# Kernel tuning notes

Measured on AMD Instinct MI355X. Metric: run time of the kernel, lower is better.

The kernel has to match this reference:

```python
import jax, jax.numpy as jnp
import numpy as np

B, N, D_IN, D_OUT = 8, 2048, 256, 256
BN_EPS = 1e-5
SELU_ALPHA = 1.6732632423543772
SELU_SCALE = 1.0507009873554805


def setup_inputs() -> dict:
    key = jax.random.key(0)
    k1, k2, k3, k4 = jax.random.split(key, 4)
    lim_lin = 1.0 / np.sqrt(D_IN)
    return {
        "x": jax.random.normal(k1, (B, N, D_IN), dtype=jnp.float32),
        "w_map": jax.random.uniform(k2, (D_IN,), jnp.float32, -lim_lin, lim_lin),
        "w_att": jax.random.uniform(k3, (D_OUT, D_IN), jnp.float32, -lim_lin, lim_lin),
        "w_res": jax.random.uniform(k4, (D_OUT, D_IN), jnp.float32, -lim_lin, lim_lin),
        "gamma": jnp.ones((D_OUT,), jnp.float32),
        "beta": jnp.zeros((D_OUT,), jnp.float32),
    }


def _selu(x):
    x_clamped = jnp.clip(x, -10.0, 10.0)
    return SELU_SCALE * jnp.where(x > 0, x, SELU_ALPHA * (jnp.exp(x_clamped) - 1.0))


def reference(x, w_map, w_att, w_res, gamma, beta):
    # scores[b,i,j] = sum_d w_map[d] * x[b,i,d] * x[b,j,d]  (== W_map(x_i*x_j))
    scores = jnp.einsum("bid,bjd->bij", x * w_map, x)  # [B,N,N]
    attn = jax.nn.softmax(scores, axis=-1)
    aggregated = jnp.einsum("bij,bjd->bid", attn, x)  # [B,N,D]
    out = aggregated @ w_att.T + x @ w_res.T  # [B,N,D_OUT]
    # BatchNorm1d in training mode: stats over (batch, nodes) per channel, biased var
    mean = jnp.mean(out, axis=(0, 1))
    var = jnp.mean(jnp.square(out - mean), axis=(0, 1))
    out = (out - mean) * jax.lax.rsqrt(var + BN_EPS) * gamma + beta
    return _selu(out)
```

## Files before the change

kernel.cpp:

```cpp
#include <hip/hip_runtime.h>
#include <hip/hip_bf16.h>


typedef __attribute__((ext_vector_type(8))) short  bf16x8;
typedef __attribute__((ext_vector_type(4))) float  f32x4;

#define MFMA16(a, b, c) __builtin_amdgcn_mfma_f32_16x16x32_bf16((a), (b), (c), 0, 0, 0)

constexpr int   NB = 8, NN = 2048, ND = 256;
constexpr int   ROWS = NB * NN;
constexpr float BN_EPS = 1e-5f;
constexpr float SELU_ALPHA = 1.6732632423543772f;
constexpr float SELU_SCALE = 1.0507009873554805f;

__device__ __forceinline__ unsigned short f2bf(float f) {
  union { float f; unsigned int u; } v; v.f = f;
  unsigned int u = v.u;
  u += 0x7FFFu + ((u >> 16) & 1u);
  return (unsigned short)(u >> 16);
}
__device__ __forceinline__ float bf2f(unsigned short h) {
  union { float f; unsigned int u; } v; v.u = ((unsigned int)h) << 16;
  return v.f;
}

__device__ __forceinline__ void async_copy16(const unsigned short* g, unsigned short* l) {
  __builtin_amdgcn_global_load_lds(
      (const __attribute__((address_space(1))) void*)g,
      (__attribute__((address_space(3))) void*)l, 16, 0, 0);
}

__global__ __launch_bounds__(256) void k0_prep(const float* __restrict__ x,
                                               const float* __restrict__ w_att,
                                               const float* __restrict__ w_res,
                                               unsigned short* __restrict__ Xr,
                                               unsigned short* __restrict__ Xt,
                                               unsigned short* __restrict__ WC,
                                               float* __restrict__ sums) {
  __shared__ unsigned short Ls[32 * 264];
  const int t = threadIdx.x;
  if (blockIdx.x >= 512) {
    const int bid = blockIdx.x - 512;
    if (bid == 0 && t < 128)
      ((float4*)sums)[t] = make_float4(0.f, 0.f, 0.f, 0.f);
    int f = (bid * 256 + t) * 8;
    int c = f >> 9, k = f & 511;
    const float* src = (k < 256) ? (w_att + c * 256 + k) : (w_res + c * 256 + (k - 256));
    float4 a = *(const float4*)src;
    float4 b = *(const float4*)(src + 4);
    union { unsigned short s[8]; uint4 v; } o;
    o.s[0] = f2bf(a.x); o.s[1] = f2bf(a.y); o.s[2] = f2bf(a.z); o.s[3] = f2bf(a.w);
    o.s[4] = f2bf(b.x); o.s[5] = f2bf(b.y); o.s[6] = f2bf(b.z); o.s[7] = f2bf(b.w);
    *(uint4*)(WC + f) = o.v;
    return;
  }
  const int b = blockIdx.x & 7, rt = blockIdx.x >> 3;
  const int grb = b * NN + rt * 32;
  const int c = (t & 31) * 8, r0 = t >> 5;
#pragma unroll
  for (int q = 0; q < 4; ++q) {
    int r = r0 + q * 8;
    const float* xp = x + (size_t)(grb + r) * 256 + c;
    float4 a = *(const float4*)xp;
    float4 d = *(const float4*)(xp + 4);
    union { unsigned short s[8]; uint4 v; } xb;
    xb.s[0] = f2bf(a.x); xb.s[1] = f2bf(a.y); xb.s[2] = f2bf(a.z); xb.s[3] = f2bf(a.w);
    xb.s[4] = f2bf(d.x); xb.s[5] = f2bf(d.y); xb.s[6] = f2bf(d.z); xb.s[7] = f2bf(d.w);
    *(uint4*)(Xr + (size_t)(grb + r) * 256 + c) = xb.v;
    *(uint4*)&Ls[r * 264 + c] = xb.v;
  }
  __syncthreads();
  unsigned short* dst = Xt + ((size_t)b * 256 + t) * 2048 + rt * 32;
#pragma unroll
  for (int k = 0; k < 4; ++k) {
    union { unsigned short s[8]; uint4 v; } o;
#pragma unroll
    for (int j = 0; j < 8; ++j) o.s[j] = Ls[(k * 8 + j) * 264 + t];
    *(uint4*)(dst + k * 8) = o.v;
  }
}

__global__ __launch_bounds__(512, 2) void k1_attn(const float* __restrict__ w_map,
                                                  const unsigned short* __restrict__ Xr,
                                                  const unsigned short* __restrict__ Xt,
                                                  const unsigned short* __restrict__ WC,
                                                  float* __restrict__ out,
                                                  float* __restrict__ sums) {
  __shared__ unsigned short Ks[2][2][32 * 256];
  __shared__ unsigned short Vt[2][2][256 * 32];
  __shared__ unsigned short Psw[8][16 * 40];
  __shared__ float Lb[64];

  const int t = threadIdx.x;
  const int w = t >> 6, lane = t & 63, l15 = lane & 15, quad = lane >> 4;
  const int g = w >> 2, wg = w & 3;
  const int b = blockIdx.x & 7, it = blockIdx.x >> 3;
  const int gib = b * NN + it * 64;
  const unsigned short* Xtb = Xt + (size_t)b * 256 * 2048;
  const unsigned short* Xrb = Xr + (size_t)b * NN * 256;
  const int jgbase = g * 1024;

  int ksOff[4], vtOff[4];
#pragma unroll
  for (int q = 0; q < 4; ++q) {
    int j = wg * 8 + q * 2 + (lane >> 5);
    int ck = (lane & 31) ^ (j & 7);
    ksOff[q] = j * 256 + ck * 8;
    int d = wg * 64 + q * 16 + (lane >> 2);
    int cv = (lane & 3) ^ ((d >> 1) & 3);
    vtOff[q] = d * 2048 + cv * 8;
  }
  const int ldsOff = wg * 2048 + lane * 8;

  bf16x8 qf[8];
  {
    const unsigned short* xrow = Xrb + (size_t)(it * 64 + wg * 16 + l15) * 256;
#pragma unroll
    for (int kc = 0; kc < 8; ++kc) {
      bf16x8 xb = *(const bf16x8*)(xrow + kc * 32 + quad * 8);
      const float* wp = w_map + kc * 32 + quad * 8;
      float4 w0 = *(const float4*)wp, w1 = *(const float4*)(wp + 4);
      float wv[8] = {w0.x, w0.y, w0.z, w0.w, w1.x, w1.y, w1.z, w1.w};
      bf16x8 q;
#pragma unroll
      for (int i = 0; i < 8; ++i)
        q[i] = (short)f2bf(bf2f((unsigned short)xb[i]) * wv[i]);
      qf[kc] = q;
    }
  }

  const f32x4 fz = {0.f, 0.f, 0.f, 0.f};
  f32x4 oacc[16];
#pragma unroll
  for (int i = 0; i < 16; ++i) oacc[i] = fz;
  f32x4 oL = fz;

  bf16x8 onesFrag;
  {
    short o1 = (l15 == 0) ? (short)0x3F80 : (short)0;
#pragma unroll
    for (int i = 0; i < 8; ++i) onesFrag[i] = o1;
  }

#pragma unroll
  for (int q = 0; q < 4; ++q)
    async_copy16(Xrb + (size_t)jgbase * 256 + ksOff[q], &Ks[g][0][ldsOff + q * 512]);
#pragma unroll
  for (int q = 0; q < 4; ++q)
    async_copy16(Xtb + jgbase + vtOff[q], &Vt[g][0][ldsOff + q * 512]);

  for (int jt = 0; jt < 32; ++jt) {
    const int cur = jt & 1;
    __syncthreads();
    if (jt < 31) {
      const int jb1 = jgbase + (jt + 1) * 32;
#pragma unroll
      for (int q = 0; q < 4; ++q)
        async_copy16(Xrb + (size_t)jb1 * 256 + ksOff[q], &Ks[g][cur ^ 1][ldsOff + q * 512]);
#pragma unroll
      for (int q = 0; q < 4; ++q)
        async_copy16(Xtb + jb1 + vtOff[q], &Vt[g][cur ^ 1][ldsOff + q * 512]);
    }
#pragma unroll
    for (int jm = 0; jm < 2; ++jm) {
      const int j = jm * 16 + l15;
      f32x4 s = fz;
#pragma unroll
      for (int kc = 0; kc < 8; ++kc) {
        int ckk = kc * 4 + quad;
        bf16x8 kf = *(const bf16x8*)&Ks[g][cur][j * 256 + ((ckk ^ (j & 7)) * 8)];
        s = MFMA16(kf, qf[kc], s);
      }
      ushort4 pk;
      pk.x = f2bf(__expf(s[0])); pk.y = f2bf(__expf(s[1]));
      pk.z = f2bf(__expf(s[2])); pk.w = f2bf(__expf(s[3]));
      *(ushort4*)&Psw[w][l15 * 40 + jm * 16 + quad * 4] = pk;
    }
    bf16x8 af = *(const bf16x8*)&Psw[w][l15 * 40 + quad * 8];
#pragma unroll
    for (int nti = 0; nti < 16; ++nti) {
      const int d = nti * 16 + l15;
      bf16x8 vf = *(const bf16x8*)&Vt[g][cur][d * 32 + ((quad ^ ((d >> 1) & 3)) * 8)];
      oacc[nti] = MFMA16(af, vf, oacc[nti]);
    }
    oL = MFMA16(af, onesFrag, oL);
  }

  __syncthreads();
  float* Obuf = (float*)&Ks[0][0][0];
  unsigned short* Agg = &Vt[0][0][0];
  if (g == 1) {
#pragma unroll
    for (int nti = 0; nti < 16; ++nti)
#pragma unroll
      for (int r = 0; r < 4; ++r) {
        int row = quad * 4 + r;
        Obuf[wg * 4096 + row * 256 + (((nti + quad) & 15) << 4) + l15] = oacc[nti][r];
      }
    if (l15 == 0) {
#pragma unroll
      for (int r = 0; r < 4; ++r) Lb[wg * 16 + quad * 4 + r] = oL[r];
    }
  }
  __syncthreads();
  if (g == 0) {
    float ls[4];
#pragma unroll
    for (int r = 0; r < 4; ++r) ls[r] = Lb[wg * 16 + quad * 4 + r];
#pragma unroll
    for (int nti = 0; nti < 16; ++nti)
#pragma unroll
      for (int r = 0; r < 4; ++r) {
        int row = quad * 4 + r;
        oacc[nti][r] += Obuf[wg * 4096 + row * 256 + (((nti + quad) & 15) << 4) + l15];
      }
    float li[4];
#pragma unroll
    for (int r = 0; r < 4; ++r)
      li[r] = 1.0f / (__shfl(oL[r], lane & 48) + ls[r]);
#pragma unroll
    for (int nti = 0; nti < 16; ++nti)
#pragma unroll
      for (int r = 0; r < 4; ++r)
        Agg[(wg * 16 + quad * 4 + r) * 264 + nti * 16 + l15] =
            f2bf(oacc[nti][r] * li[r]);
  }
  __syncthreads();

  f32x4 eacc[2][4];
#pragma unroll
  for (int i = 0; i < 2; ++i)
#pragma unroll
    for (int j = 0; j < 4; ++j) eacc[i][j] = fz;

#pragma unroll
  for (int kc = 0; kc < 16; ++kc) {
    bf16x8 bf0 = *(const bf16x8*)(WC + (size_t)(w * 32 + l15) * 512 + kc * 32 + quad * 8);
    bf16x8 bf1 = *(const bf16x8*)(WC + (size_t)(w * 32 + 16 + l15) * 512 + kc * 32 + quad * 8);
#pragma unroll
    for (int rt = 0; rt < 4; ++rt) {
      bf16x8 af;
      if (kc < 8)
        af = *(const bf16x8*)&Agg[(rt * 16 + l15) * 264 + kc * 32 + quad * 8];
      else
        af = *(const bf16x8*)(Xrb + (size_t)(it * 64 + rt * 16 + l15) * 256 +
                              (kc - 8) * 32 + quad * 8);
      eacc[0][rt] = MFMA16(af, bf0, eacc[0][rt]);
      eacc[1][rt] = MFMA16(af, bf1, eacc[1][rt]);
    }
  }
#pragma unroll
  for (int nt = 0; nt < 2; ++nt) {
    float a = 0.f, b2 = 0.f;
#pragma unroll
    for (int rt = 0; rt < 4; ++rt)
#pragma unroll
      for (int r = 0; r < 4; ++r) {
        float v = eacc[nt][rt][r];
        a += v; b2 += v * v;
      }
    a += __shfl_xor(a, 16);  a += __shfl_xor(a, 32);
    b2 += __shfl_xor(b2, 16); b2 += __shfl_xor(b2, 32);
    if (quad == 0) {
      int ci = w * 32 + nt * 16 + l15;
      atomicAdd(&sums[ci], a);
      atomicAdd(&sums[256 + ci], b2);
    }
  }
#pragma unroll
  for (int nt = 0; nt < 2; ++nt) {
    const int gcol = w * 32 + nt * 16 + l15;
#pragma unroll
    for (int rt = 0; rt < 4; ++rt)
#pragma unroll
      for (int r = 0; r < 4; ++r) {
        const int grow = gib + rt * 16 + quad * 4 + r;
        out[(size_t)grow * 256 + gcol] = eacc[nt][rt][r];
      }
  }
}

__global__ __launch_bounds__(256) void k4_bn_selu(float* __restrict__ out,
                                                  const float* __restrict__ sums,
                                                  const float* __restrict__ gamma,
                                                  const float* __restrict__ beta) {
  __shared__ float sc[256], sh[256];
  const int t = threadIdx.x;
  {
    const float inv_m = 1.0f / 16384.0f;
    float mean = sums[t] * inv_m;
    float var = sums[256 + t] * inv_m - mean * mean;
    float s = rsqrtf(var + BN_EPS) * gamma[t];
    sc[t] = s;
    sh[t] = beta[t] - mean * s;
  }
  __syncthreads();
  int f = (blockIdx.x * 256 + t) * 8;
  int c = f & 255;
  float4 v0 = *(const float4*)(out + f);
  float4 v1 = *(const float4*)(out + f + 4);
  float vv[8] = {v0.x, v0.y, v0.z, v0.w, v1.x, v1.y, v1.z, v1.w};
#pragma unroll
  for (int k = 0; k < 8; ++k) {
    int ch = c + k;
    float y = vv[k] * sc[ch] + sh[ch];
    float yc = fminf(fmaxf(y, -10.f), 10.f);
    float r = (y > 0.f) ? y : (SELU_ALPHA * (expf(yc) - 1.0f));
    vv[k] = SELU_SCALE * r;
  }
  float4 o0 = {vv[0], vv[1], vv[2], vv[3]};
  float4 o1 = {vv[4], vv[5], vv[6], vv[7]};
  *(float4*)(out + f) = o0;
  *(float4*)(out + f + 4) = o1;
}

extern "C" void kernel_launch(void* const* d_in, const int* in_sizes, int n_in,
                              void* d_out, int out_size, void* d_ws, size_t ws_size,
                              hipStream_t stream) {
  const float* x     = (const float*)d_in[0];
  const float* w_map = (const float*)d_in[1];
  const float* w_att = (const float*)d_in[2];
  const float* w_res = (const float*)d_in[3];
  const float* gamma = (const float*)d_in[4];
  const float* beta  = (const float*)d_in[5];
  float* out = (float*)d_out;

  unsigned short* Xr = (unsigned short*)d_ws;
  unsigned short* Xt = Xr + (size_t)ROWS * 256;
  unsigned short* WC = Xt + (size_t)NB * 256 * 2048;
  float* sums = (float*)(WC + 256 * 512);

  k0_prep<<<576, 256, 0, stream>>>(x, w_att, w_res, Xr, Xt, WC, sums);
  k1_attn<<<256, 512, 0, stream>>>(w_map, Xr, Xt, WC, out, sums);
  k4_bn_selu<<<2048, 256, 0, stream>>>(out, sums, gamma, beta);
}
```

Measured before the change: 167.4 us.

## Transpose MFMA outputs for vector stores and stage query tile in LDS

Swaps MFMA operand order in the PV and output projection so each lane holds four consecutive columns. This allows float4 global stores of the output and 16-byte LDS exchanges in the cross-group reduction, which is split into two halves to fit the buffer. The query-row X tile is prefetched into LDS during the last iteration and WC fragments are preloaded into registers. Launch bounds drop to one block per SM minimum, which raises register pressure and may reduce occupancy; the BN-stat shuffle pattern also changes to match the new layout.

```diff
diff --git a/kernel.cpp b/kernel.cpp
--- a/kernel.cpp
+++ b/kernel.cpp
@@ -80,16 +80,16 @@
   }
 }
 
-__global__ __launch_bounds__(512, 2) void k1_attn(const float* __restrict__ w_map,
+__global__ __launch_bounds__(512, 1) void k1_attn(const float* __restrict__ w_map,
                                                   const unsigned short* __restrict__ Xr,
                                                   const unsigned short* __restrict__ Xt,
                                                   const unsigned short* __restrict__ WC,
                                                   float* __restrict__ out,
                                                   float* __restrict__ sums) {
-  __shared__ unsigned short Ks[2][2][32 * 256];
-  __shared__ unsigned short Vt[2][2][256 * 32];
+  __shared__ unsigned short Ks2[2][2][32 * 256];
+  __shared__ unsigned short Vt2[2][2][256 * 32];
   __shared__ unsigned short Psw[8][16 * 40];
-  __shared__ float Lb[64];
+  __shared__ float LbG[2][64];
 
   const int t = threadIdx.x;
   const int w = t >> 6, lane = t & 63, l15 = lane & 15, quad = lane >> 4;
@@ -100,7 +100,7 @@
   const unsigned short* Xrb = Xr + (size_t)b * NN * 256;
   const int jgbase = g * 1024;
 
-  int ksOff[4], vtOff[4];
+  int ksOff[4], vtOff[4], xsOff[4];
 #pragma unroll
   for (int q = 0; q < 4; ++q) {
     int j = wg * 8 + q * 2 + (lane >> 5);
@@ -109,6 +109,8 @@
     int d = wg * 64 + q * 16 + (lane >> 2);
     int cv = (lane & 3) ^ ((d >> 1) & 3);
     vtOff[q] = d * 2048 + cv * 8;
+    int xr = w * 8 + q * 2 + (lane >> 5);
+    xsOff[q] = (it * 64 + xr) * 256 + (((lane & 31) ^ (xr & 7)) * 8);
   }
   const int ldsOff = wg * 2048 + lane * 8;
 
@@ -144,10 +146,10 @@
 
 #pragma unroll
   for (int q = 0; q < 4; ++q)
-    async_copy16(Xrb + (size_t)jgbase * 256 + ksOff[q], &Ks[g][0][ldsOff + q * 512]);
+    async_copy16(Xrb + (size_t)jgbase * 256 + ksOff[q], &Ks2[0][g][ldsOff + q * 512]);
 #pragma unroll
   for (int q = 0; q < 4; ++q)
-    async_copy16(Xtb + jgbase + vtOff[q], &Vt[g][0][ldsOff + q * 512]);
+    async_copy16(Xtb + jgbase + vtOff[q], &Vt2[0][g][ldsOff + q * 512]);
 
   for (int jt = 0; jt < 32; ++jt) {
     const int cur = jt & 1;
@@ -156,10 +158,15 @@
       const int jb1 = jgbase + (jt + 1) * 32;
 #pragma unroll
       for (int q = 0; q < 4; ++q)
-        async_copy16(Xrb + (size_t)jb1 * 256 + ksOff[q], &Ks[g][cur ^ 1][ldsOff + q * 512]);
+        async_copy16(Xrb + (size_t)jb1 * 256 + ksOff[q], &Ks2[cur ^ 1][g][ldsOff + q * 512]);
 #pragma unroll
       for (int q = 0; q < 4; ++q)
-        async_copy16(Xtb + jb1 + vtOff[q], &Vt[g][cur ^ 1][ldsOff + q * 512]);
+        async_copy16(Xtb + jb1 + vtOff[q], &Vt2[cur ^ 1][g][ldsOff + q * 512]);
+    } else {
+#pragma unroll
+      for (int q = 0; q < 4; ++q)
+        async_copy16(Xrb + (size_t)xsOff[q],
+                     &Ks2[0][0][(w * 8 + q * 2) * 256 + lane * 8]);
     }
 #pragma unroll
     for (int jm = 0; jm < 2; ++jm) {
@@ -168,7 +175,7 @@
 #pragma unroll
       for (int kc = 0; kc < 8; ++kc) {
         int ckk = kc * 4 + quad;
-        bf16x8 kf = *(const bf16x8*)&Ks[g][cur][j * 256 + ((ckk ^ (j & 7)) * 8)];
+        bf16x8 kf = *(const bf16x8*)&Ks2[cur][g][j * 256 + ((ckk ^ (j & 7)) * 8)];
         s = MFMA16(kf, qf[kc], s);
       }
       ushort4 pk;
@@ -180,50 +187,76 @@
 #pragma unroll
     for (int nti = 0; nti < 16; ++nti) {
       const int d = nti * 16 + l15;
-      bf16x8 vf = *(const bf16x8*)&Vt[g][cur][d * 32 + ((quad ^ ((d >> 1) & 3)) * 8)];
-      oacc[nti] = MFMA16(af, vf, oacc[nti]);
+      bf16x8 vf = *(const bf16x8*)&Vt2[cur][g][d * 32 + ((quad ^ ((d >> 1) & 3)) * 8)];
+      oacc[nti] = MFMA16(vf, af, oacc[nti]);
     }
     oL = MFMA16(af, onesFrag, oL);
   }
 
-  __syncthreads();
-  float* Obuf = (float*)&Ks[0][0][0];
-  unsigned short* Agg = &Vt[0][0][0];
+  unsigned short* Xs  = &Ks2[0][0][0];
+  unsigned short* Agg = &Ks2[1][0][0];
+  float* OB = (float*)&Vt2[0][0][0];
+
+  if (l15 == 0) {
+#pragma unroll
+    for (int r = 0; r < 4; ++r) LbG[g][wg * 16 + quad * 4 + r] = oL[r];
+  }
   if (g == 1) {
-#pragma unroll
-    for (int nti = 0; nti < 16; ++nti)
-#pragma unroll
-      for (int r = 0; r < 4; ++r) {
-        int row = quad * 4 + r;
-        Obuf[wg * 4096 + row * 256 + (((nti + quad) & 15) << 4) + l15] = oacc[nti][r];
-      }
-    if (l15 == 0) {
-#pragma unroll
-      for (int r = 0; r < 4; ++r) Lb[wg * 16 + quad * 4 + r] = oL[r];
-    }
-  }
-  __syncthreads();
+    const int q = wg * 16 + l15;
+#pragma unroll
+    for (int nti = 0; nti < 8; ++nti) {
+      int dd = nti * 16 + quad * 4;
+      *(f32x4*)&OB[q * 128 + (dd ^ ((q & 7) * 4))] = oacc[nti];
+    }
+  }
+  __syncthreads();
+
+  bf16x8 wcf[2][16];
+#pragma unroll
+  for (int nt = 0; nt < 2; ++nt)
+#pragma unroll
+    for (int kc = 0; kc < 16; ++kc)
+      wcf[nt][kc] = *(const bf16x8*)(WC + (size_t)(w * 32 + nt * 16 + l15) * 512 +
+                                     kc * 32 + quad * 8);
+
   if (g == 0) {
-    float ls[4];
-#pragma unroll
-    for (int r = 0; r < 4; ++r) ls[r] = Lb[wg * 16 + quad * 4 + r];
-#pragma unroll
-    for (int nti = 0; nti < 16; ++nti)
-#pragma unroll
-      for (int r = 0; r < 4; ++r) {
-        int row = quad * 4 + r;
-        oacc[nti][r] += Obuf[wg * 4096 + row * 256 + (((nti + quad) & 15) << 4) + l15];
-      }
-    float li[4];
-#pragma unroll
-    for (int r = 0; r < 4; ++r)
-      li[r] = 1.0f / (__shfl(oL[r], lane & 48) + ls[r]);
-#pragma unroll
-    for (int nti = 0; nti < 16; ++nti)
-#pragma unroll
-      for (int r = 0; r < 4; ++r)
-        Agg[(wg * 16 + quad * 4 + r) * 264 + nti * 16 + l15] =
-            f2bf(oacc[nti][r] * li[r]);
+    const int q = wg * 16 + l15;
+#pragma unroll
+    for (int nti = 0; nti < 8; ++nti) {
+      int dd = nti * 16 + quad * 4;
+      f32x4 p = *(const f32x4*)&OB[q * 128 + (dd ^ ((q & 7) * 4))];
+#pragma unroll
+      for (int r = 0; r < 4; ++r) oacc[nti][r] += p[r];
+    }
+  }
+  __syncthreads();
+  if (g == 1) {
+    const int q = wg * 16 + l15;
+#pragma unroll
+    for (int nti = 8; nti < 16; ++nti) {
+      int dd = (nti - 8) * 16 + quad * 4;
+      *(f32x4*)&OB[q * 128 + (dd ^ ((q & 7) * 4))] = oacc[nti];
+    }
+  }
+  __syncthreads();
+  if (g == 0) {
+    const int q = wg * 16 + l15;
+#pragma unroll
+    for (int nti = 8; nti < 16; ++nti) {
+      int dd = (nti - 8) * 16 + quad * 4;
+      f32x4 p = *(const f32x4*)&OB[q * 128 + (dd ^ ((q & 7) * 4))];
+#pragma unroll
+      for (int r = 0; r < 4; ++r) oacc[nti][r] += p[r];
+    }
+    float li = 1.0f / (LbG[0][q] + LbG[1][q]);
+#pragma unroll
+    for (int nti = 0; nti < 16; ++nti) {
+      ushort4 pk;
+      pk.x = f2bf(oacc[nti][0] * li); pk.y = f2bf(oacc[nti][1] * li);
+      pk.z = f2bf(oacc[nti][2] * li); pk.w = f2bf(oacc[nti][3] * li);
+      int chunk = nti * 2 + (quad >> 1);
+      *(ushort4*)&Agg[q * 256 + ((chunk ^ (q & 7)) * 8) + (quad & 1) * 4] = pk;
+    }
   }
   __syncthreads();
 
@@ -235,49 +268,50 @@
 
 #pragma unroll
   for (int kc = 0; kc < 16; ++kc) {
-    bf16x8 bf0 = *(const bf16x8*)(WC + (size_t)(w * 32 + l15) * 512 + kc * 32 + quad * 8);
-    bf16x8 bf1 = *(const bf16x8*)(WC + (size_t)(w * 32 + 16 + l15) * 512 + kc * 32 + quad * 8);
+    bf16x8 bfr[4];
 #pragma unroll
     for (int rt = 0; rt < 4; ++rt) {
-      bf16x8 af;
+      const int row = rt * 16 + l15;
       if (kc < 8)
-        af = *(const bf16x8*)&Agg[(rt * 16 + l15) * 264 + kc * 32 + quad * 8];
+        bfr[rt] = *(const bf16x8*)&Agg[row * 256 + (((kc * 4 + quad) ^ (row & 7)) * 8)];
       else
-        af = *(const bf16x8*)(Xrb + (size_t)(it * 64 + rt * 16 + l15) * 256 +
-                              (kc - 8) * 32 + quad * 8);
-      eacc[0][rt] = MFMA16(af, bf0, eacc[0][rt]);
-      eacc[1][rt] = MFMA16(af, bf1, eacc[1][rt]);
-    }
-  }
-#pragma unroll
-  for (int nt = 0; nt < 2; ++nt) {
-    float a = 0.f, b2 = 0.f;
-#pragma unroll
-    for (int rt = 0; rt < 4; ++rt)
-#pragma unroll
-      for (int r = 0; r < 4; ++r) {
+        bfr[rt] = *(const bf16x8*)&Xs[row * 256 + ((((kc - 8) * 4 + quad) ^ (row & 7)) * 8)];
+    }
+#pragma unroll
+    for (int nt = 0; nt < 2; ++nt)
+#pragma unroll
+      for (int rt = 0; rt < 4; ++rt)
+        eacc[nt][rt] = MFMA16(wcf[nt][kc], bfr[rt], eacc[nt][rt]);
+  }
+
+#pragma unroll
+  for (int nt = 0; nt < 2; ++nt)
+#pragma unroll
+    for (int r = 0; r < 4; ++r) {
+      float a = 0.f, b2 = 0.f;
+#pragma unroll
+      for (int rt = 0; rt < 4; ++rt) {
         float v = eacc[nt][rt][r];
         a += v; b2 += v * v;
       }
-    a += __shfl_xor(a, 16);  a += __shfl_xor(a, 32);
-    b2 += __shfl_xor(b2, 16); b2 += __shfl_xor(b2, 32);
-    if (quad == 0) {
-      int ci = w * 32 + nt * 16 + l15;
-      atomicAdd(&sums[ci], a);
-      atomicAdd(&sums[256 + ci], b2);
-    }
-  }
-#pragma unroll
-  for (int nt = 0; nt < 2; ++nt) {
-    const int gcol = w * 32 + nt * 16 + l15;
-#pragma unroll
-    for (int rt = 0; rt < 4; ++rt)
-#pragma unroll
-      for (int r = 0; r < 4; ++r) {
-        const int grow = gib + rt * 16 + quad * 4 + r;
-        out[(size_t)grow * 256 + gcol] = eacc[nt][rt][r];
+      a += __shfl_xor(a, 1); a += __shfl_xor(a, 2);
+      a += __shfl_xor(a, 4); a += __shfl_xor(a, 8);
+      b2 += __shfl_xor(b2, 1); b2 += __shfl_xor(b2, 2);
+      b2 += __shfl_xor(b2, 4); b2 += __shfl_xor(b2, 8);
+      if (l15 == 0) {
+        int ch = w * 32 + nt * 16 + quad * 4 + r;
+        atomicAdd(&sums[ch], a);
+        atomicAdd(&sums[256 + ch], b2);
       }
-  }
+    }
+
+#pragma unroll
+  for (int nt = 0; nt < 2; ++nt)
+#pragma unroll
+    for (int rt = 0; rt < 4; ++rt) {
+      float4 v = {eacc[nt][rt][0], eacc[nt][rt][1], eacc[nt][rt][2], eacc[nt][rt][3]};
+      *(float4*)&out[(size_t)(gib + rt * 16 + l15) * 256 + w * 32 + nt * 16 + quad * 4] = v;
+    }
 }
 
 __global__ __launch_bounds__(256) void k4_bn_selu(float* __restrict__ out,
```

Measured after the change: 178.8 us. 6.8% more time.
